# Performance work log

Hardware: AMD Instinct MI355X
Metric: run time of the kernel (lower is better)

## Reference

```python
import jax, jax.numpy as jnp
import numpy as np

N_NODES = 100000
N_EDGES = 1200000
IN_F = 64
OUT_F = 64


def setup_inputs() -> dict:
    key = jax.random.key(0)
    ks = jax.random.split(key, 8)
    rows = jax.random.randint(ks[0], (N_EDGES,), 0, N_NODES)
    cols = jax.random.randint(ks[1], (N_EDGES,), 0, N_NODES)
    vals = jax.random.uniform(ks[2], (N_EDGES,), dtype=jnp.float32)
    features = jax.random.normal(ks[3], (N_NODES, IN_F), dtype=jnp.float32)
    W1 = jax.random.normal(ks[4], (IN_F, OUT_F), dtype=jnp.float32) / np.sqrt(IN_F)
    b1 = jax.random.normal(ks[5], (OUT_F,), dtype=jnp.float32) * 0.01
    W2 = jax.random.normal(ks[6], (IN_F, OUT_F), dtype=jnp.float32) / np.sqrt(IN_F)
    b2 = jax.random.normal(ks[7], (OUT_F,), dtype=jnp.float32) * 0.01
    return {"rows": rows, "cols": cols, "vals": vals, "features": features,
            "W1": W1, "b1": b1, "W2": W2, "b2": b2}


def _spmm(rows, cols, vals, x):
    # y[r] = sum_{e: rows[e]==r} vals[e] * x[cols[e]]  -- COO SpMM via gather + segment_sum
    msgs = vals[:, None] * x[cols]  # [E, F]
    return jax.ops.segment_sum(msgs, rows, num_segments=N_NODES)


def reference(rows, cols, vals, features, W1, b1, W2, b2):
    # L1 = laplacian + selfLoop(identity)  =>  L1 @ X = L @ X + X
    agg1 = _spmm(rows, cols, vals, features) + features          # [N, inF]
    inter_feature = features * features                           # elementwise square
    agg2 = _spmm(rows, cols, vals, inter_feature)                 # [N, inF]
    part1 = agg1 @ W1 + b1                                        # linear
    part2 = agg2 @ W2 + b2                                        # interActTransform
    return part1 + part2
```

## Files before the change

### kernel.cpp

```cpp
#include <hip/hip_runtime.h>


#define ROWS_PER_BUCKET 128
#define ROW_SHIFT 7
#define NBUCK_PAD 784
#define SCAN_T 196
#define CAP 2048
#define CHUNK 4096
#define EPT 16
#define MAXB 2048
#define COL_BITS 17
#define COL_MASK 0x1FFFF
#define OVF_CAP 65536

typedef __attribute__((ext_vector_type(8))) short bf16x8;
typedef __attribute__((ext_vector_type(4))) float f32x4;

__device__ __forceinline__ unsigned short f2bf(float x) {
    unsigned u = __float_as_uint(x);
    unsigned r = (u + 0x7FFFu + ((u >> 16) & 1u)) >> 16;
    return (unsigned short)r;
}
__device__ __forceinline__ float bf2f(unsigned short h) {
    return __uint_as_float(((unsigned)h) << 16);
}

__global__ __launch_bounds__(256) void node_transform(
    const float* __restrict__ X, const float* __restrict__ W1,
    const float* __restrict__ b1, const float* __restrict__ W2,
    const float* __restrict__ b2, unsigned short* __restrict__ Yb,
    float* __restrict__ Z, int n_nodes,
    int* __restrict__ gcursor, int* __restrict__ ovf_count)
{
    const int tid = threadIdx.x;

    if (gcursor) {
        int gi = blockIdx.x * 256 + tid;
        if (gi < NBUCK_PAD) gcursor[gi] = gi * CAP;
        if (gi == 0) *ovf_count = 0;
    }

    const int lane = tid & 63;
    const int wave = tid >> 6;
    const int lg = lane >> 4;
    const int lr = lane & 15;

    const int base = blockIdx.x * 128 + wave * 32;

    bf16x8 bw1[2][4];
    bf16x8 bw2[2][4];
#pragma unroll
    for (int ks = 0; ks < 2; ++ks) {
#pragma unroll
        for (int cf = 0; cf < 4; ++cf) {
            const int col = cf * 16 + lr;
            const int k0 = ks * 32 + lg * 8;
            bf16x8 t1, t2;
#pragma unroll
            for (int j = 0; j < 8; ++j) {
                t1[j] = (short)f2bf(W1[(k0 + j) * 64 + col]);
                t2[j] = (short)f2bf(W2[(k0 + j) * 64 + col]);
            }
            bw1[ks][cf] = t1;
            bw2[ks][cf] = t2;
        }
    }

    f32x4 acc1[2][4];
    f32x4 acc2[2][4];
#pragma unroll
    for (int rf = 0; rf < 2; ++rf)
#pragma unroll
        for (int cf = 0; cf < 4; ++cf) {
            acc1[rf][cf] = (f32x4){0.f, 0.f, 0.f, 0.f};
            acc2[rf][cf] = (f32x4){0.f, 0.f, 0.f, 0.f};
        }

#pragma unroll
    for (int rf = 0; rf < 2; ++rf) {
        const int row = base + rf * 16 + lr;
        const bool rok = row < n_nodes;
        const float* xp = X + (size_t)row * 64 + lg * 8;
#pragma unroll
        for (int ks = 0; ks < 2; ++ks) {
            float xv[8];
            if (rok) {
                float4 v0 = *(const float4*)(xp + ks * 32);
                float4 v1 = *(const float4*)(xp + ks * 32 + 4);
                xv[0] = v0.x; xv[1] = v0.y; xv[2] = v0.z; xv[3] = v0.w;
                xv[4] = v1.x; xv[5] = v1.y; xv[6] = v1.z; xv[7] = v1.w;
            } else {
#pragma unroll
                for (int j = 0; j < 8; ++j) xv[j] = 0.f;
            }
            bf16x8 a, q;
#pragma unroll
            for (int j = 0; j < 8; ++j) {
                a[j] = (short)f2bf(xv[j]);
                float s = xv[j] * xv[j];
                q[j] = (short)f2bf(s);
            }
#pragma unroll
            for (int cf = 0; cf < 4; ++cf) {
                acc1[rf][cf] = __builtin_amdgcn_mfma_f32_16x16x32_bf16(
                    a, bw1[ks][cf], acc1[rf][cf], 0, 0, 0);
                acc2[rf][cf] = __builtin_amdgcn_mfma_f32_16x16x32_bf16(
                    q, bw2[ks][cf], acc2[rf][cf], 0, 0, 0);
            }
        }
    }

    float bsv[4];
#pragma unroll
    for (int cf = 0; cf < 4; ++cf)
        bsv[cf] = b1[cf * 16 + lr] + b2[cf * 16 + lr];

#pragma unroll
    for (int rf = 0; rf < 2; ++rf) {
#pragma unroll
        for (int i = 0; i < 4; ++i) {
            const int row = base + rf * 16 + lg * 4 + i;
            if (row < n_nodes) {
#pragma unroll
                for (int cf = 0; cf < 4; ++cf) {
                    const float v1 = acc1[rf][cf][i];
                    const float y = v1 + acc2[rf][cf][i];
                    const float z = v1 + bsv[cf];
                    Yb[(size_t)row * 64 + cf * 16 + lr] = f2bf(y);
                    Z[(size_t)row * 64 + cf * 16 + lr] = z;
                }
            }
        }
    }
}


__global__ __launch_bounds__(256) void bin_scatter(
    const int* __restrict__ rows, const int* __restrict__ cols,
    const float* __restrict__ vals, int* __restrict__ gcursor,
    int2* __restrict__ packed, int* __restrict__ ovf_count,
    int4* __restrict__ ovf, int n_edges) {
    __shared__ int lcount[NBUCK_PAD];
    __shared__ int lstart[NBUCK_PAD];
    __shared__ int gbase[NBUCK_PAD];
    __shared__ int2 sxy[CHUNK];
    __shared__ unsigned short sbk[CHUNK];
    __shared__ int wsum[4];

    int tid = threadIdx.x;
    int eb0 = blockIdx.x * CHUNK;
    int cnt = min(CHUNK, n_edges - eb0);

    for (int k = tid; k < NBUCK_PAD; k += 256) lcount[k] = 0;
    __syncthreads();

    int eb_[EPT], ep_[EPT], ex_[EPT], ey_[EPT];
#pragma unroll
    for (int t = 0; t < EPT; ++t) {
        int i = tid + 256 * t;
        if (i < cnt) {
            int r = rows[eb0 + i];
            int b = r >> ROW_SHIFT;
            eb_[t] = b;
            ep_[t] = atomicAdd(&lcount[b], 1);
            ex_[t] = ((r & (ROWS_PER_BUCKET - 1)) << COL_BITS) | cols[eb0 + i];
            ey_[t] = __float_as_int(vals[eb0 + i]);
        } else {
            eb_[t] = -1; ep_[t] = 0; ex_[t] = 0; ey_[t] = 0;
        }
    }
    __syncthreads();

    int c0 = 0, c1 = 0, c2 = 0, c3 = 0, psum = 0;
    if (tid < SCAN_T) {
        c0 = lcount[tid * 4 + 0]; c1 = lcount[tid * 4 + 1];
        c2 = lcount[tid * 4 + 2]; c3 = lcount[tid * 4 + 3];
        psum = c0 + c1 + c2 + c3;
    }
    const int lane = tid & 63;
    const int wv = tid >> 6;
    int incl = psum;
#pragma unroll
    for (int o = 1; o < 64; o <<= 1) {
        int n = __shfl_up(incl, o);
        if (lane >= o) incl += n;
    }
    if (lane == 63) wsum[wv] = incl;
    __syncthreads();
    int wpre = 0;
#pragma unroll
    for (int w = 0; w < 3; ++w)
        if (w < wv) wpre += wsum[w];
    int base0 = wpre + incl - psum;
    if (tid < SCAN_T) {
        lstart[tid * 4 + 0] = base0;
        lstart[tid * 4 + 1] = base0 + c0;
        lstart[tid * 4 + 2] = base0 + c0 + c1;
        lstart[tid * 4 + 3] = base0 + c0 + c1 + c2;
    }
    __syncthreads();

    for (int k = tid; k < NBUCK_PAD; k += 256) {
        if (lcount[k] > 0) gbase[k] = atomicAdd(&gcursor[k], lcount[k]);
    }

#pragma unroll
    for (int t = 0; t < EPT; ++t) {
        if (eb_[t] >= 0) {
            int p = lstart[eb_[t]] + ep_[t];
            sxy[p] = make_int2(ex_[t], ey_[t]);
            sbk[p] = (unsigned short)eb_[t];
        }
    }
    __syncthreads();

    for (int i = tid; i < cnt; i += 256) {
        int b = sbk[i];
        int2 a = sxy[i];
        int dest = gbase[b] + (i - lstart[b]);
        if (dest < (b + 1) * CAP) {
            packed[dest] = a;
        } else {
            int p = atomicAdd(ovf_count, 1);
            if (p < OVF_CAP)
                ovf[p] = make_int4(b * ROWS_PER_BUCKET + (a.x >> COL_BITS),
                                   a.x & COL_MASK, a.y, 0);
        }
    }
}

__global__ __launch_bounds__(256) void bucket_gather_quads(
    const int* __restrict__ gcursor, const int2* __restrict__ packed,
    const unsigned short* __restrict__ Yb, float* __restrict__ out,
    int n_nodes) {
    __shared__ int2 sxy[MAXB];
    __shared__ int hist[ROWS_PER_BUCKET];
    __shared__ int chs[ROWS_PER_BUCKET];
    __shared__ int chc[ROWS_PER_BUCKET];

    int tid = threadIdx.x;
    int bucket = blockIdx.x >> 1;
    int rhalf = (blockIdx.x & 1) * 64;
    int fquad = tid & 15;
    int grp = tid >> 4;
    int s = bucket * CAP;
    int e = min(gcursor[bucket], s + CAP);
    int row0 = bucket * ROWS_PER_BUCKET;
    const uint2* __restrict__ Y64 = (const uint2*)Yb;

    for (int cb = s; cb < e; cb += MAXB) {
        int cnt = min(MAXB, e - cb);

        if (tid < ROWS_PER_BUCKET) hist[tid] = 0;
        __syncthreads();

        for (int i = tid; i < cnt; i += 256)
            atomicAdd(&hist[packed[cb + i].x >> COL_BITS], 1);
        __syncthreads();

        if (tid < ROWS_PER_BUCKET) chs[tid] = hist[tid];
        __syncthreads();
#pragma unroll
        for (int o = 1; o < ROWS_PER_BUCKET; o <<= 1) {
            int t = 0;
            if (tid < ROWS_PER_BUCKET && tid >= o) t = chs[tid - o];
            __syncthreads();
            if (tid < ROWS_PER_BUCKET) chs[tid] += t;
            __syncthreads();
        }
        if (tid < ROWS_PER_BUCKET) {
            int excl = chs[tid] - hist[tid];
            chs[tid] = excl;
            chc[tid] = excl;
        }
        __syncthreads();

        for (int i = tid; i < cnt; i += 256) {
            int2 a = packed[cb + i];
            int p = atomicAdd(&chc[a.x >> COL_BITS], 1);
            sxy[p] = a;
        }
        __syncthreads();

        for (int rr = 0; rr < 4; ++rr) {
            int r = rhalf + grp * 4 + rr;
            int rc = hist[r];
            int node = row0 + r;
            if (rc == 0 || node >= n_nodes) continue;
            int rs = chs[r];
            float a0 = 0.f, a1 = 0.f, a2 = 0.f, a3 = 0.f;
            int j = 0;
            for (; j + 4 <= rc; j += 4) {
                int2 e0 = sxy[rs + j + 0], e1 = sxy[rs + j + 1];
                int2 e2 = sxy[rs + j + 2], e3 = sxy[rs + j + 3];
                uint2 u0 = Y64[(size_t)(e0.x & COL_MASK) * 16 + fquad];
                uint2 u1 = Y64[(size_t)(e1.x & COL_MASK) * 16 + fquad];
                uint2 u2 = Y64[(size_t)(e2.x & COL_MASK) * 16 + fquad];
                uint2 u3 = Y64[(size_t)(e3.x & COL_MASK) * 16 + fquad];
                float v0 = __int_as_float(e0.y), v1 = __int_as_float(e1.y);
                float v2 = __int_as_float(e2.y), v3 = __int_as_float(e3.y);
                a0 = fmaf(v0, __uint_as_float(u0.x << 16), a0);
                a1 = fmaf(v0, __uint_as_float(u0.x & 0xFFFF0000u), a1);
                a2 = fmaf(v0, __uint_as_float(u0.y << 16), a2);
                a3 = fmaf(v0, __uint_as_float(u0.y & 0xFFFF0000u), a3);
                a0 = fmaf(v1, __uint_as_float(u1.x << 16), a0);
                a1 = fmaf(v1, __uint_as_float(u1.x & 0xFFFF0000u), a1);
                a2 = fmaf(v1, __uint_as_float(u1.y << 16), a2);
                a3 = fmaf(v1, __uint_as_float(u1.y & 0xFFFF0000u), a3);
                a0 = fmaf(v2, __uint_as_float(u2.x << 16), a0);
                a1 = fmaf(v2, __uint_as_float(u2.x & 0xFFFF0000u), a1);
                a2 = fmaf(v2, __uint_as_float(u2.y << 16), a2);
                a3 = fmaf(v2, __uint_as_float(u2.y & 0xFFFF0000u), a3);
                a0 = fmaf(v3, __uint_as_float(u3.x << 16), a0);
                a1 = fmaf(v3, __uint_as_float(u3.x & 0xFFFF0000u), a1);
                a2 = fmaf(v3, __uint_as_float(u3.y << 16), a2);
                a3 = fmaf(v3, __uint_as_float(u3.y & 0xFFFF0000u), a3);
            }
            for (; j < rc; ++j) {
                int2 e0 = sxy[rs + j];
                uint2 u0 = Y64[(size_t)(e0.x & COL_MASK) * 16 + fquad];
                float v0 = __int_as_float(e0.y);
                a0 = fmaf(v0, __uint_as_float(u0.x << 16), a0);
                a1 = fmaf(v0, __uint_as_float(u0.x & 0xFFFF0000u), a1);
                a2 = fmaf(v0, __uint_as_float(u0.y << 16), a2);
                a3 = fmaf(v0, __uint_as_float(u0.y & 0xFFFF0000u), a3);
            }
            float4* op = (float4*)(out + (size_t)node * 64 + fquad * 4);
            float4 o = *op;
            o.x += a0; o.y += a1; o.z += a2; o.w += a3;
            *op = o;
        }
        __syncthreads();
    }
}

__global__ __launch_bounds__(256) void overflow_scatter(
    const int* __restrict__ ovf_count, const int4* __restrict__ ovf,
    const unsigned short* __restrict__ Yb, float* __restrict__ out) {
    int cnt = min(*ovf_count, OVF_CAP);
    long long total = (long long)cnt * 64;
    for (long long i = blockIdx.x * 256 + threadIdx.x; i < total;
         i += (long long)gridDim.x * 256) {
        int e = (int)(i >> 6), f = (int)(i & 63);
        int4 a = ovf[e];
        atomicAdd(&out[(size_t)a.x * 64 + f],
                  __int_as_float(a.z) * bf2f(Yb[(size_t)a.y * 64 + f]));
    }
}


__global__ __launch_bounds__(256) void edge_scatter(
    const int* __restrict__ rows, const int* __restrict__ cols,
    const float* __restrict__ vals, const unsigned short* __restrict__ Yb,
    float* __restrict__ out, int n_edges)
{
    int t = blockIdx.x * 256 + threadIdx.x;
    int e = t >> 4;
    int f = (t & 15) << 2;
    if (e >= n_edges) return;
    int r = rows[e];
    int c = cols[e];
    float v = vals[e];
    const unsigned short* y = Yb + (size_t)c * 64 + f;
    float* o = out + (size_t)r * 64 + f;
    atomicAdd(o + 0, v * bf2f(y[0]));
    atomicAdd(o + 1, v * bf2f(y[1]));
    atomicAdd(o + 2, v * bf2f(y[2]));
    atomicAdd(o + 3, v * bf2f(y[3]));
}

extern "C" void kernel_launch(void* const* d_in, const int* in_sizes, int n_in,
                              void* d_out, int out_size, void* d_ws, size_t ws_size,
                              hipStream_t stream) {
    const int*   rows = (const int*)d_in[0];
    const int*   cols = (const int*)d_in[1];
    const float* vals = (const float*)d_in[2];
    const float* X    = (const float*)d_in[3];
    const float* W1   = (const float*)d_in[4];
    const float* b1   = (const float*)d_in[5];
    const float* W2   = (const float*)d_in[6];
    const float* b2   = (const float*)d_in[7];
    float* out = (float*)d_out;

    const int n_edges = in_sizes[0];
    const int n_nodes = in_sizes[3] / 64;
    const int nbuck = (n_nodes + ROWS_PER_BUCKET - 1) / ROWS_PER_BUCKET;

    char* ws = (char*)d_ws;
    size_t o_Yb     = 0;
    size_t o_packed = o_Yb + (size_t)n_nodes * 64 * 2;
    size_t o_ovf    = o_packed + (size_t)NBUCK_PAD * CAP * 8;
    size_t o_gcurs  = o_ovf + (size_t)OVF_CAP * 16;
    size_t o_ovfcnt = o_gcurs + NBUCK_PAD * 4;
    size_t need     = o_ovfcnt + 16;

    unsigned short* Yb = (unsigned short*)(ws + o_Yb);

    const bool fastpath =
        ws_size >= need && nbuck <= NBUCK_PAD && n_nodes <= (1 << COL_BITS);

    int2* packed  = (int2*)(ws + o_packed);
    int4* ovf     = (int4*)(ws + o_ovf);
    int*  gcursor = fastpath ? (int*)(ws + o_gcurs) : (int*)0;
    int*  ovfcnt  = (int*)(ws + o_ovfcnt);

    int nblocks = (n_nodes + 127) / 128;
    node_transform<<<nblocks, 256, 0, stream>>>(X, W1, b1, W2, b2, Yb, out,
                                                n_nodes, gcursor, ovfcnt);

    if (fastpath) {
        int eb = (n_edges + CHUNK - 1) / CHUNK;
        bin_scatter<<<eb, 256, 0, stream>>>(rows, cols, vals, gcursor, packed,
                                            ovfcnt, ovf, n_edges);
        bucket_gather_quads<<<nbuck * 2, 256, 0, stream>>>(gcursor, packed, Yb,
                                                           out, n_nodes);
        overflow_scatter<<<128, 256, 0, stream>>>(ovfcnt, ovf, Yb, out);
    } else {
        long long threads = (long long)n_edges * 16;
        int eblocks = (int)((threads + 255) / 256);
        edge_scatter<<<eblocks, 256, 0, stream>>>(rows, cols, vals, Yb, out, n_edges);
    }
}
```

Measured before the change: 160.8 us.

## Merge node transform and edge binning into one heterogeneous launch

The dense node transform (MFMA) and the edge bin-scatter kernel are fused into a single grid where the first blocks do the transform and the rest do binning, so the two independent phases run concurrently. Cursor initialization moves into a tiny separate kernel because binning can no longer depend on the transform kernel to initialize it. The fused kernel carries the binning kernel's large shared memory allocation in every block, which can reduce occupancy for the transform blocks, and it adds an extra small launch.

Measured after the change: 162.4 us. No clear change (+1.0%).

```diff
diff --git a/kernel.cpp b/kernel.cpp
--- a/kernel.cpp
+++ b/kernel.cpp
@@ -25,121 +25,23 @@
     return __uint_as_float(((unsigned)h) << 16);
 }
 
-__global__ __launch_bounds__(256) void node_transform(
+__global__ __launch_bounds__(256) void cursor_init(
+    int* __restrict__ gcursor, int* __restrict__ ovf_count) {
+    int i = blockIdx.x * 256 + threadIdx.x;
+    if (i < NBUCK_PAD) gcursor[i] = i * CAP;
+    if (i == 0) *ovf_count = 0;
+}
+
+__global__ __launch_bounds__(256) void nt_scatter(
     const float* __restrict__ X, const float* __restrict__ W1,
     const float* __restrict__ b1, const float* __restrict__ W2,
     const float* __restrict__ b2, unsigned short* __restrict__ Yb,
-    float* __restrict__ Z, int n_nodes,
-    int* __restrict__ gcursor, int* __restrict__ ovf_count)
-{
-    const int tid = threadIdx.x;
-
-    if (gcursor) {
-        int gi = blockIdx.x * 256 + tid;
-        if (gi < NBUCK_PAD) gcursor[gi] = gi * CAP;
-        if (gi == 0) *ovf_count = 0;
-    }
-
-    const int lane = tid & 63;
-    const int wave = tid >> 6;
-    const int lg = lane >> 4;
-    const int lr = lane & 15;
-
-    const int base = blockIdx.x * 128 + wave * 32;
-
-    bf16x8 bw1[2][4];
-    bf16x8 bw2[2][4];
-#pragma unroll
-    for (int ks = 0; ks < 2; ++ks) {
-#pragma unroll
-        for (int cf = 0; cf < 4; ++cf) {
-            const int col = cf * 16 + lr;
-            const int k0 = ks * 32 + lg * 8;
-            bf16x8 t1, t2;
-#pragma unroll
-            for (int j = 0; j < 8; ++j) {
-                t1[j] = (short)f2bf(W1[(k0 + j) * 64 + col]);
-                t2[j] = (short)f2bf(W2[(k0 + j) * 64 + col]);
-            }
-            bw1[ks][cf] = t1;
-            bw2[ks][cf] = t2;
-        }
-    }
-
-    f32x4 acc1[2][4];
-    f32x4 acc2[2][4];
-#pragma unroll
-    for (int rf = 0; rf < 2; ++rf)
-#pragma unroll
-        for (int cf = 0; cf < 4; ++cf) {
-            acc1[rf][cf] = (f32x4){0.f, 0.f, 0.f, 0.f};
-            acc2[rf][cf] = (f32x4){0.f, 0.f, 0.f, 0.f};
-        }
-
-#pragma unroll
-    for (int rf = 0; rf < 2; ++rf) {
-        const int row = base + rf * 16 + lr;
-        const bool rok = row < n_nodes;
-        const float* xp = X + (size_t)row * 64 + lg * 8;
-#pragma unroll
-        for (int ks = 0; ks < 2; ++ks) {
-            float xv[8];
-            if (rok) {
-                float4 v0 = *(const float4*)(xp + ks * 32);
-                float4 v1 = *(const float4*)(xp + ks * 32 + 4);
-                xv[0] = v0.x; xv[1] = v0.y; xv[2] = v0.z; xv[3] = v0.w;
-                xv[4] = v1.x; xv[5] = v1.y; xv[6] = v1.z; xv[7] = v1.w;
-            } else {
-#pragma unroll
-                for (int j = 0; j < 8; ++j) xv[j] = 0.f;
-            }
-            bf16x8 a, q;
-#pragma unroll
-            for (int j = 0; j < 8; ++j) {
-                a[j] = (short)f2bf(xv[j]);
-                float s = xv[j] * xv[j];
-                q[j] = (short)f2bf(s);
-            }
-#pragma unroll
-            for (int cf = 0; cf < 4; ++cf) {
-                acc1[rf][cf] = __builtin_amdgcn_mfma_f32_16x16x32_bf16(
-                    a, bw1[ks][cf], acc1[rf][cf], 0, 0, 0);
-                acc2[rf][cf] = __builtin_amdgcn_mfma_f32_16x16x32_bf16(
-                    q, bw2[ks][cf], acc2[rf][cf], 0, 0, 0);
-            }
-        }
-    }
-
-    float bsv[4];
-#pragma unroll
-    for (int cf = 0; cf < 4; ++cf)
-        bsv[cf] = b1[cf * 16 + lr] + b2[cf * 16 + lr];
-
-#pragma unroll
-    for (int rf = 0; rf < 2; ++rf) {
-#pragma unroll
-        for (int i = 0; i < 4; ++i) {
-            const int row = base + rf * 16 + lg * 4 + i;
-            if (row < n_nodes) {
-#pragma unroll
-                for (int cf = 0; cf < 4; ++cf) {
-                    const float v1 = acc1[rf][cf][i];
-                    const float y = v1 + acc2[rf][cf][i];
-                    const float z = v1 + bsv[cf];
-                    Yb[(size_t)row * 64 + cf * 16 + lr] = f2bf(y);
-                    Z[(size_t)row * 64 + cf * 16 + lr] = z;
-                }
-            }
-        }
-    }
-}
-
-
-__global__ __launch_bounds__(256) void bin_scatter(
+    float* __restrict__ Z, int n_nodes, int nt_blocks,
     const int* __restrict__ rows, const int* __restrict__ cols,
     const float* __restrict__ vals, int* __restrict__ gcursor,
     int2* __restrict__ packed, int* __restrict__ ovf_count,
-    int4* __restrict__ ovf, int n_edges) {
+    int4* __restrict__ ovf, int n_edges)
+{
     __shared__ int lcount[NBUCK_PAD];
     __shared__ int lstart[NBUCK_PAD];
     __shared__ int gbase[NBUCK_PAD];
@@ -147,9 +49,106 @@
     __shared__ unsigned short sbk[CHUNK];
     __shared__ int wsum[4];
 
-    int tid = threadIdx.x;
-    int eb0 = blockIdx.x * CHUNK;
+    const int tid = threadIdx.x;
+
+    if (blockIdx.x < (unsigned)nt_blocks) {
+        const int lane = tid & 63;
+        const int wave = tid >> 6;
+        const int lg = lane >> 4;
+        const int lr = lane & 15;
+        const int base = blockIdx.x * 128 + wave * 32;
+
+        bf16x8 bw1[2][4];
+        bf16x8 bw2[2][4];
+#pragma unroll
+        for (int ks = 0; ks < 2; ++ks) {
+#pragma unroll
+            for (int cf = 0; cf < 4; ++cf) {
+                const int col = cf * 16 + lr;
+                const int k0 = ks * 32 + lg * 8;
+                bf16x8 t1, t2;
+#pragma unroll
+                for (int j = 0; j < 8; ++j) {
+                    t1[j] = (short)f2bf(W1[(k0 + j) * 64 + col]);
+                    t2[j] = (short)f2bf(W2[(k0 + j) * 64 + col]);
+                }
+                bw1[ks][cf] = t1;
+                bw2[ks][cf] = t2;
+            }
+        }
+
+        f32x4 acc1[2][4];
+        f32x4 acc2[2][4];
+#pragma unroll
+        for (int rf = 0; rf < 2; ++rf)
+#pragma unroll
+            for (int cf = 0; cf < 4; ++cf) {
+                acc1[rf][cf] = (f32x4){0.f, 0.f, 0.f, 0.f};
+                acc2[rf][cf] = (f32x4){0.f, 0.f, 0.f, 0.f};
+            }
+
+#pragma unroll
+        for (int rf = 0; rf < 2; ++rf) {
+            const int row = base + rf * 16 + lr;
+            const bool rok = row < n_nodes;
+            const float* xp = X + (size_t)row * 64 + lg * 8;
+#pragma unroll
+            for (int ks = 0; ks < 2; ++ks) {
+                float xv[8];
+                if (rok) {
+                    float4 v0 = *(const float4*)(xp + ks * 32);
+                    float4 v1 = *(const float4*)(xp + ks * 32 + 4);
+                    xv[0] = v0.x; xv[1] = v0.y; xv[2] = v0.z; xv[3] = v0.w;
+                    xv[4] = v1.x; xv[5] = v1.y; xv[6] = v1.z; xv[7] = v1.w;
+                } else {
+#pragma unroll
+                    for (int j = 0; j < 8; ++j) xv[j] = 0.f;
+                }
+                bf16x8 a, q;
+#pragma unroll
+                for (int j = 0; j < 8; ++j) {
+                    a[j] = (short)f2bf(xv[j]);
+                    float s = xv[j] * xv[j];
+                    q[j] = (short)f2bf(s);
+                }
+#pragma unroll
+                for (int cf = 0; cf < 4; ++cf) {
+                    acc1[rf][cf] = __builtin_amdgcn_mfma_f32_16x16x32_bf16(
+                        a, bw1[ks][cf], acc1[rf][cf], 0, 0, 0);
+                    acc2[rf][cf] = __builtin_amdgcn_mfma_f32_16x16x32_bf16(
+                        q, bw2[ks][cf], acc2[rf][cf], 0, 0, 0);
+                }
+            }
+        }
+
+        float bsv[4];
+#pragma unroll
+        for (int cf = 0; cf < 4; ++cf)
+            bsv[cf] = b1[cf * 16 + lr] + b2[cf * 16 + lr];
+
+#pragma unroll
+        for (int rf = 0; rf < 2; ++rf) {
+#pragma unroll
+            for (int i = 0; i < 4; ++i) {
+                const int row = base + rf * 16 + lg * 4 + i;
+                if (row < n_nodes) {
+#pragma unroll
+                    for (int cf = 0; cf < 4; ++cf) {
+                        const float v1 = acc1[rf][cf][i];
+                        const float y = v1 + acc2[rf][cf][i];
+                        const float z = v1 + bsv[cf];
+                        Yb[(size_t)row * 64 + cf * 16 + lr] = f2bf(y);
+                        Z[(size_t)row * 64 + cf * 16 + lr] = z;
+                    }
+                }
+            }
+        }
+        return;
+    }
+
+    int eb0 = (blockIdx.x - nt_blocks) * CHUNK;
     int cnt = min(CHUNK, n_edges - eb0);
+    if (cnt <= 0) return;
 
     for (int k = tid; k < NBUCK_PAD; k += 256) lcount[k] = 0;
     __syncthreads();
@@ -401,21 +400,24 @@
 
     int2* packed  = (int2*)(ws + o_packed);
     int4* ovf     = (int4*)(ws + o_ovf);
-    int*  gcursor = fastpath ? (int*)(ws + o_gcurs) : (int*)0;
+    int*  gcursor = (int*)(ws + o_gcurs);
     int*  ovfcnt  = (int*)(ws + o_ovfcnt);
 
     int nblocks = (n_nodes + 127) / 128;
-    node_transform<<<nblocks, 256, 0, stream>>>(X, W1, b1, W2, b2, Yb, out,
-                                                n_nodes, gcursor, ovfcnt);
 
     if (fastpath) {
         int eb = (n_edges + CHUNK - 1) / CHUNK;
-        bin_scatter<<<eb, 256, 0, stream>>>(rows, cols, vals, gcursor, packed,
-                                            ovfcnt, ovf, n_edges);
+        cursor_init<<<(NBUCK_PAD + 255) / 256, 256, 0, stream>>>(gcursor, ovfcnt);
+        nt_scatter<<<nblocks + eb, 256, 0, stream>>>(
+            X, W1, b1, W2, b2, Yb, out, n_nodes, nblocks,
+            rows, cols, vals, gcursor, packed, ovfcnt, ovf, n_edges);
         bucket_gather_quads<<<nbuck * 2, 256, 0, stream>>>(gcursor, packed, Yb,
                                                            out, n_nodes);
         overflow_scatter<<<128, 256, 0, stream>>>(ovfcnt, ovf, Yb, out);
     } else {
+        nt_scatter<<<nblocks, 256, 0, stream>>>(
+            X, W1, b1, W2, b2, Yb, out, n_nodes, nblocks,
+            rows, cols, vals, (int*)0, (int2*)0, (int*)0, (int4*)0, 0);
         long long threads = (long long)n_edges * 16;
         int eblocks = (int)((threads + 255) / 256);
         edge_scatter<<<eblocks, 256, 0, stream>>>(rows, cols, vals, Yb, out, n_edges);
```

## Precompute per-row edge histogram globally and simplify bucket gather to half-bucket sort

Applied to the files above, without the earlier changes.

Per-row edge counts are now built with global atomics in bin_scatter into a zeroed workspace histogram, instead of each gather block recomputing a shared-memory histogram with an extra pass over packed edges. Each gather block then does a wave-level shuffle scan over only its 64 rows and stages only the edges belonging to its half-bucket. This drops the per-block histogram pass and the barrier-heavy 128-wide scan. In exchange, bin_scatter performs one extra global atomic per edge, and a rarely taken per-feature global-atomic fallback is added for overflow inside the staging buffer.

After: 199.0 us. 1.24x slower.

```diff
diff --git a/kernel.cpp b/kernel.cpp
--- a/kernel.cpp
+++ b/kernel.cpp
@@ -8,7 +8,6 @@
 #define CAP 2048
 #define CHUNK 4096
 #define EPT 16
-#define MAXB 2048
 #define COL_BITS 17
 #define COL_MASK 0x1FFFF
 #define OVF_CAP 65536
@@ -30,7 +29,8 @@
     const float* __restrict__ b1, const float* __restrict__ W2,
     const float* __restrict__ b2, unsigned short* __restrict__ Yb,
     float* __restrict__ Z, int n_nodes,
-    int* __restrict__ gcursor, int* __restrict__ ovf_count)
+    int* __restrict__ gcursor, int* __restrict__ ovf_count,
+    int* __restrict__ ghist)
 {
     const int tid = threadIdx.x;
 
@@ -38,6 +38,8 @@
         int gi = blockIdx.x * 256 + tid;
         if (gi < NBUCK_PAD) gcursor[gi] = gi * CAP;
         if (gi == 0) *ovf_count = 0;
+        for (int k = gi; k < NBUCK_PAD * ROWS_PER_BUCKET; k += gridDim.x * 256)
+            ghist[k] = 0;
     }
 
     const int lane = tid & 63;
@@ -139,7 +141,7 @@
     const int* __restrict__ rows, const int* __restrict__ cols,
     const float* __restrict__ vals, int* __restrict__ gcursor,
     int2* __restrict__ packed, int* __restrict__ ovf_count,
-    int4* __restrict__ ovf, int n_edges) {
+    int4* __restrict__ ovf, int* __restrict__ ghist, int n_edges) {
     __shared__ int lcount[NBUCK_PAD];
     __shared__ int lstart[NBUCK_PAD];
     __shared__ int gbase[NBUCK_PAD];
@@ -163,6 +165,7 @@
             int b = r >> ROW_SHIFT;
             eb_[t] = b;
             ep_[t] = atomicAdd(&lcount[b], 1);
+            atomicAdd(&ghist[r], 1);
             ex_[t] = ((r & (ROWS_PER_BUCKET - 1)) << COL_BITS) | cols[eb0 + i];
             ey_[t] = __float_as_int(vals[eb0 + i]);
         } else {
@@ -229,108 +232,107 @@
     }
 }
 
-__global__ __launch_bounds__(256) void bucket_gather_quads(
+__global__ __launch_bounds__(256) void bucket_gather_half(
     const int* __restrict__ gcursor, const int2* __restrict__ packed,
-    const unsigned short* __restrict__ Yb, float* __restrict__ out,
-    int n_nodes) {
-    __shared__ int2 sxy[MAXB];
-    __shared__ int hist[ROWS_PER_BUCKET];
-    __shared__ int chs[ROWS_PER_BUCKET];
-    __shared__ int chc[ROWS_PER_BUCKET];
+    const int* __restrict__ ghist, const unsigned short* __restrict__ Yb,
+    float* __restrict__ out, int n_nodes) {
+    __shared__ int2 sxy[CAP];
+    __shared__ int chs[64];
+    __shared__ int chc[64];
 
     int tid = threadIdx.x;
     int bucket = blockIdx.x >> 1;
-    int rhalf = (blockIdx.x & 1) * 64;
+    int half = blockIdx.x & 1;
+    int rhalf = half * 64;
     int fquad = tid & 15;
     int grp = tid >> 4;
     int s = bucket * CAP;
     int e = min(gcursor[bucket], s + CAP);
+    int cnt = e - s;
     int row0 = bucket * ROWS_PER_BUCKET;
     const uint2* __restrict__ Y64 = (const uint2*)Yb;
 
-    for (int cb = s; cb < e; cb += MAXB) {
-        int cnt = min(MAXB, e - cb);
-
-        if (tid < ROWS_PER_BUCKET) hist[tid] = 0;
-        __syncthreads();
-
-        for (int i = tid; i < cnt; i += 256)
-            atomicAdd(&hist[packed[cb + i].x >> COL_BITS], 1);
-        __syncthreads();
-
-        if (tid < ROWS_PER_BUCKET) chs[tid] = hist[tid];
-        __syncthreads();
-#pragma unroll
-        for (int o = 1; o < ROWS_PER_BUCKET; o <<= 1) {
-            int t = 0;
-            if (tid < ROWS_PER_BUCKET && tid >= o) t = chs[tid - o];
-            __syncthreads();
-            if (tid < ROWS_PER_BUCKET) chs[tid] += t;
-            __syncthreads();
-        }
-        if (tid < ROWS_PER_BUCKET) {
-            int excl = chs[tid] - hist[tid];
-            chs[tid] = excl;
-            chc[tid] = excl;
-        }
-        __syncthreads();
-
-        for (int i = tid; i < cnt; i += 256) {
-            int2 a = packed[cb + i];
-            int p = atomicAdd(&chc[a.x >> COL_BITS], 1);
-            sxy[p] = a;
-        }
-        __syncthreads();
-
-        for (int rr = 0; rr < 4; ++rr) {
-            int r = rhalf + grp * 4 + rr;
-            int rc = hist[r];
-            int node = row0 + r;
-            if (rc == 0 || node >= n_nodes) continue;
-            int rs = chs[r];
-            float a0 = 0.f, a1 = 0.f, a2 = 0.f, a3 = 0.f;
-            int j = 0;
-            for (; j + 4 <= rc; j += 4) {
-                int2 e0 = sxy[rs + j + 0], e1 = sxy[rs + j + 1];
-                int2 e2 = sxy[rs + j + 2], e3 = sxy[rs + j + 3];
-                uint2 u0 = Y64[(size_t)(e0.x & COL_MASK) * 16 + fquad];
-                uint2 u1 = Y64[(size_t)(e1.x & COL_MASK) * 16 + fquad];
-                uint2 u2 = Y64[(size_t)(e2.x & COL_MASK) * 16 + fquad];
-                uint2 u3 = Y64[(size_t)(e3.x & COL_MASK) * 16 + fquad];
-                float v0 = __int_as_float(e0.y), v1 = __int_as_float(e1.y);
-                float v2 = __int_as_float(e2.y), v3 = __int_as_float(e3.y);
-                a0 = fmaf(v0, __uint_as_float(u0.x << 16), a0);
-                a1 = fmaf(v0, __uint_as_float(u0.x & 0xFFFF0000u), a1);
-                a2 = fmaf(v0, __uint_as_float(u0.y << 16), a2);
-                a3 = fmaf(v0, __uint_as_float(u0.y & 0xFFFF0000u), a3);
-                a0 = fmaf(v1, __uint_as_float(u1.x << 16), a0);
-                a1 = fmaf(v1, __uint_as_float(u1.x & 0xFFFF0000u), a1);
-                a2 = fmaf(v1, __uint_as_float(u1.y << 16), a2);
-                a3 = fmaf(v1, __uint_as_float(u1.y & 0xFFFF0000u), a3);
-                a0 = fmaf(v2, __uint_as_float(u2.x << 16), a0);
-                a1 = fmaf(v2, __uint_as_float(u2.x & 0xFFFF0000u), a1);
-                a2 = fmaf(v2, __uint_as_float(u2.y << 16), a2);
-                a3 = fmaf(v2, __uint_as_float(u2.y & 0xFFFF0000u), a3);
-                a0 = fmaf(v3, __uint_as_float(u3.x << 16), a0);
-                a1 = fmaf(v3, __uint_as_float(u3.x & 0xFFFF0000u), a1);
-                a2 = fmaf(v3, __uint_as_float(u3.y << 16), a2);
-                a3 = fmaf(v3, __uint_as_float(u3.y & 0xFFFF0000u), a3);
-            }
-            for (; j < rc; ++j) {
-                int2 e0 = sxy[rs + j];
-                uint2 u0 = Y64[(size_t)(e0.x & COL_MASK) * 16 + fquad];
-                float v0 = __int_as_float(e0.y);
-                a0 = fmaf(v0, __uint_as_float(u0.x << 16), a0);
-                a1 = fmaf(v0, __uint_as_float(u0.x & 0xFFFF0000u), a1);
-                a2 = fmaf(v0, __uint_as_float(u0.y << 16), a2);
-                a3 = fmaf(v0, __uint_as_float(u0.y & 0xFFFF0000u), a3);
-            }
-            float4* op = (float4*)(out + (size_t)node * 64 + fquad * 4);
-            float4 o = *op;
-            o.x += a0; o.y += a1; o.z += a2; o.w += a3;
-            *op = o;
-        }
-        __syncthreads();
+    if (tid < 64) {
+        int h = ghist[row0 + rhalf + tid];
+        int incl = h;
+#pragma unroll
+        for (int o = 1; o < 64; o <<= 1) {
+            int n = __shfl_up(incl, o);
+            if (tid >= o) incl += n;
+        }
+        chs[tid] = incl - h;
+        chc[tid] = incl - h;
+    }
+    __syncthreads();
+
+    for (int i = tid; i < cnt; i += 256) {
+        int2 a = packed[s + i];
+        int lr = a.x >> COL_BITS;
+        if ((lr >> 6) == half) {
+            int p = atomicAdd(&chc[lr & 63], 1);
+            if (p < CAP) {
+                sxy[p] = a;
+            } else {
+                int node = row0 + lr;
+                int c = a.x & COL_MASK;
+                float v = __int_as_float(a.y);
+                if (node < n_nodes)
+                    for (int f = 0; f < 64; ++f)
+                        atomicAdd(&out[(size_t)node * 64 + f],
+                                  v * bf2f(Yb[(size_t)c * 64 + f]));
+            }
+        }
+    }
+    __syncthreads();
+
+    for (int rr = 0; rr < 4; ++rr) {
+        int lr = grp * 4 + rr;
+        int node = row0 + rhalf + lr;
+        int rs = chs[lr];
+        int re = min(chc[lr], CAP);
+        int rc = re - rs;
+        if (rc <= 0 || node >= n_nodes) continue;
+        float a0 = 0.f, a1 = 0.f, a2 = 0.f, a3 = 0.f;
+        int j = 0;
+        for (; j + 4 <= rc; j += 4) {
+            int2 e0 = sxy[rs + j + 0], e1 = sxy[rs + j + 1];
+            int2 e2 = sxy[rs + j + 2], e3 = sxy[rs + j + 3];
+            uint2 u0 = Y64[(size_t)(e0.x & COL_MASK) * 16 + fquad];
+            uint2 u1 = Y64[(size_t)(e1.x & COL_MASK) * 16 + fquad];
+            uint2 u2 = Y64[(size_t)(e2.x & COL_MASK) * 16 + fquad];
+            uint2 u3 = Y64[(size_t)(e3.x & COL_MASK) * 16 + fquad];
+            float v0 = __int_as_float(e0.y), v1 = __int_as_float(e1.y);
+            float v2 = __int_as_float(e2.y), v3 = __int_as_float(e3.y);
+            a0 = fmaf(v0, __uint_as_float(u0.x << 16), a0);
+            a1 = fmaf(v0, __uint_as_float(u0.x & 0xFFFF0000u), a1);
+            a2 = fmaf(v0, __uint_as_float(u0.y << 16), a2);
+            a3 = fmaf(v0, __uint_as_float(u0.y & 0xFFFF0000u), a3);
+            a0 = fmaf(v1, __uint_as_float(u1.x << 16), a0);
+            a1 = fmaf(v1, __uint_as_float(u1.x & 0xFFFF0000u), a1);
+            a2 = fmaf(v1, __uint_as_float(u1.y << 16), a2);
+            a3 = fmaf(v1, __uint_as_float(u1.y & 0xFFFF0000u), a3);
+            a0 = fmaf(v2, __uint_as_float(u2.x << 16), a0);
+            a1 = fmaf(v2, __uint_as_float(u2.x & 0xFFFF0000u), a1);
+            a2 = fmaf(v2, __uint_as_float(u2.y << 16), a2);
+            a3 = fmaf(v2, __uint_as_float(u2.y & 0xFFFF0000u), a3);
+            a0 = fmaf(v3, __uint_as_float(u3.x << 16), a0);
+            a1 = fmaf(v3, __uint_as_float(u3.x & 0xFFFF0000u), a1);
+            a2 = fmaf(v3, __uint_as_float(u3.y << 16), a2);
+            a3 = fmaf(v3, __uint_as_float(u3.y & 0xFFFF0000u), a3);
+        }
+        for (; j < rc; ++j) {
+            int2 e0 = sxy[rs + j];
+            uint2 u0 = Y64[(size_t)(e0.x & COL_MASK) * 16 + fquad];
+            float v0 = __int_as_float(e0.y);
+            a0 = fmaf(v0, __uint_as_float(u0.x << 16), a0);
+            a1 = fmaf(v0, __uint_as_float(u0.x & 0xFFFF0000u), a1);
+            a2 = fmaf(v0, __uint_as_float(u0.y << 16), a2);
+            a3 = fmaf(v0, __uint_as_float(u0.y & 0xFFFF0000u), a3);
+        }
+        float4* op = (float4*)(out + (size_t)node * 64 + fquad * 4);
+        float4 o = *op;
+        o.x += a0; o.y += a1; o.z += a2; o.w += a3;
+        *op = o;
     }
 }
 
@@ -392,7 +394,8 @@
     size_t o_ovf    = o_packed + (size_t)NBUCK_PAD * CAP * 8;
     size_t o_gcurs  = o_ovf + (size_t)OVF_CAP * 16;
     size_t o_ovfcnt = o_gcurs + NBUCK_PAD * 4;
-    size_t need     = o_ovfcnt + 16;
+    size_t o_ghist  = o_ovfcnt + 16;
+    size_t need     = o_ghist + (size_t)NBUCK_PAD * ROWS_PER_BUCKET * 4;
 
     unsigned short* Yb = (unsigned short*)(ws + o_Yb);
 
@@ -403,17 +406,18 @@
     int4* ovf     = (int4*)(ws + o_ovf);
     int*  gcursor = fastpath ? (int*)(ws + o_gcurs) : (int*)0;
     int*  ovfcnt  = (int*)(ws + o_ovfcnt);
+    int*  ghist   = (int*)(ws + o_ghist);
 
     int nblocks = (n_nodes + 127) / 128;
     node_transform<<<nblocks, 256, 0, stream>>>(X, W1, b1, W2, b2, Yb, out,
-                                                n_nodes, gcursor, ovfcnt);
+                                                n_nodes, gcursor, ovfcnt, ghist);
 
     if (fastpath) {
         int eb = (n_edges + CHUNK - 1) / CHUNK;
         bin_scatter<<<eb, 256, 0, stream>>>(rows, cols, vals, gcursor, packed,
-                                            ovfcnt, ovf, n_edges);
-        bucket_gather_quads<<<nbuck * 2, 256, 0, stream>>>(gcursor, packed, Yb,
-                                                           out, n_nodes);
+                                            ovfcnt, ovf, ghist, n_edges);
+        bucket_gather_half<<<nbuck * 2, 256, 0, stream>>>(gcursor, packed, ghist,
+                                                          Yb, out, n_nodes);
         overflow_scatter<<<128, 256, 0, stream>>>(ovfcnt, ovf, Yb, out);
     } else {
         long long threads = (long long)n_edges * 16;
```
